# Optimization experiments

Measured on AMD Instinct MI355X. Metric: run time of the kernel, lower is better.

## Reference

```python
import jax, jax.numpy as jnp
import numpy as np

C, H, W = 32, 128, 128

def grid_sample_plane(plane, gx, gy):
    """PyTorch F.grid_sample(mode='bilinear', align_corners=True, padding_mode='zeros').
    plane: (C,H,W); gx,gy: (B,N) in [-1,1] (x indexes W, y indexes H).
    Returns (B,C,N)."""
    x = (gx + 1.0) * 0.5 * (W - 1)
    y = (gy + 1.0) * 0.5 * (H - 1)
    x0 = jnp.floor(x); y0 = jnp.floor(y)
    wx = x - x0; wy = y - y0
    x0i = x0.astype(jnp.int32); y0i = y0.astype(jnp.int32)
    def corner(xi, yi, w):
        valid = (xi >= 0) & (xi < W) & (yi >= 0) & (yi < H)
        xc = jnp.clip(xi, 0, W - 1); yc = jnp.clip(yi, 0, H - 1)
        v = plane[:, yc, xc]            # (C,B,N)
        return v * (w * valid)[None]
    out = (corner(x0i, y0i, (1 - wx) * (1 - wy))
           + corner(x0i + 1, y0i, wx * (1 - wy))
           + corner(x0i, y0i + 1, (1 - wx) * wy)
           + corner(x0i + 1, y0i + 1, wx * wy))   # (C,B,N)
    return jnp.transpose(out, (1, 0, 2))           # (B,C,N)


def setup_inputs() -> dict:
    key = jax.random.key(0)
    ks = jax.random.split(key, 8)
    B, N = 4, 262144
    grid_coords = jax.random.uniform(ks[0], (B, N, 3), jnp.float32, -1.0, 1.0)
    triplanes = jax.random.normal(ks[1], (3 * C, H, W), jnp.float32)
    w0 = jax.random.normal(ks[2], (128, 32), jnp.float32) * (1.0 / np.sqrt(32))
    b0 = jax.random.normal(ks[3], (128,), jnp.float32) * 0.01
    w1 = jax.random.normal(ks[4], (128, 128), jnp.float32) * (1.0 / np.sqrt(128))
    b1 = jax.random.normal(ks[5], (128,), jnp.float32) * 0.01
    w2 = jax.random.normal(ks[6], (4, 128), jnp.float32) * (1.0 / np.sqrt(128))
    b2 = jax.random.normal(ks[7], (4,), jnp.float32) * 0.01
    return {"grid_coords": grid_coords, "triplanes": triplanes,
            "w0": w0, "b0": b0, "w1": w1, "b1": b1, "w2": w2, "b2": b2}


def reference(grid_coords, triplanes, w0, b0, w1, b1, w2, b2):
    B, N, _ = grid_coords.shape
    feat_xy, feat_yz, feat_xz = jnp.split(triplanes, 3, axis=0)
    x = grid_coords[..., 0]; y = grid_coords[..., 1]; z = grid_coords[..., 2]
    # fused tri-plane gather + sum, (B,C,N)
    sampled = (grid_sample_plane(feat_xy, x, y)
               + grid_sample_plane(feat_xz, x, z)
               + grid_sample_plane(feat_yz, y, z))
    # NOTE: the original code does .reshape(batch, -1, channel) on a (B,C,1,N)
    # contiguous tensor (NOT a transpose) -- replicate that exact layout reinterpretation.
    feats = sampled.reshape(B, N, C)
    net = jax.nn.relu(feats @ w0.T + b0)
    net = jax.nn.relu(net @ w1.T + b1)
    net = jax.nn.relu(net @ w2.T + b2)            # (B,N,4)
    # raw = cat(rgb=net[...,1:4], alpha=net[...,0:1]) along channel
    raw = jnp.concatenate([net[..., 1:4], net[..., 0:1]], axis=-1)
    return raw
```

## Files before the change

### kernel.cpp

```cpp
#include <hip/hip_runtime.h>
#include <hip/hip_bf16.h>


#define C_ 32
#define HW_ (128 * 128)
#define HQS 40

typedef short s8v __attribute__((ext_vector_type(8)));
typedef float f4v __attribute__((ext_vector_type(4)));
typedef unsigned int u4v __attribute__((ext_vector_type(4)));
typedef unsigned int u2v __attribute__((ext_vector_type(2)));

__device__ __attribute__((aligned(64))) unsigned short g_planes[3 * HW_ * C_];
__device__ __attribute__((aligned(16))) unsigned short g_w0[128 * 32];
__device__ __attribute__((aligned(16))) unsigned short g_w1[128 * 128];
__device__ __attribute__((aligned(16))) unsigned short g_w2[16 * 128];
__device__ __attribute__((aligned(16))) float g_b0[128];
__device__ __attribute__((aligned(16))) float g_b1[128];
__device__ __attribute__((aligned(16))) float g_b2p[16];

template <typename TO, typename FROM>
static __device__ __forceinline__ TO bitc(FROM f) {
    union { FROM a; TO b; } u; u.a = f; return u.b;
}

template <typename V>
static __device__ __forceinline__ auto mfma_k32(V a, V b, f4v c, int)
    -> decltype(__builtin_amdgcn_mfma_f32_16x16x32_bf16(a, b, c, 0, 0, 0)) {
    return __builtin_amdgcn_mfma_f32_16x16x32_bf16(a, b, c, 0, 0, 0);
}
template <typename V>
static __device__ __forceinline__ f4v mfma_k32(V a, V b, f4v c, long) {
    typedef __bf16 b8v __attribute__((ext_vector_type(8)));
    return __builtin_amdgcn_mfma_f32_16x16x32_bf16(bitc<b8v>(a), bitc<b8v>(b), c, 0, 0, 0);
}
static __device__ __forceinline__ f4v MFMA(s8v a, s8v b, f4v c) {
    return mfma_k32(a, b, c, 0);
}

__device__ __forceinline__ unsigned short f2bf(float f) {
    union { float f; unsigned int i; } v; v.f = f;
    unsigned int r = v.i + 0x7FFFu + ((v.i >> 16) & 1u);
    return (unsigned short)(r >> 16);
}

static __device__ __forceinline__ unsigned int relu_pk(float a, float b) {
    float x = a > 0.0f ? a : 0.0f;
    float y = b > 0.0f ? b : 0.0f;
    unsigned int r;
    asm("v_cvt_pk_bf16_f32 %0, %1, %2" : "=v"(r) : "v"(x), "v"(y));
    return r;
}

__global__ __launch_bounds__(256) void prep_planes_k(const float* __restrict__ tp) {
    __shared__ float buf[32][65];
    const int tid = threadIdx.x;
    const int bid = blockIdx.x;
    const int pl  = bid >> 8;
    const int xy0 = (bid & 255) << 6;
#pragma unroll
    for (int i = 0; i < 8; ++i) {
        int idx = i * 256 + tid;
        int c = idx >> 6, x = idx & 63;
        buf[c][x] = tp[(pl * C_ + c) * HW_ + xy0 + x];
    }
    __syncthreads();
#pragma unroll
    for (int i = 0; i < 8; ++i) {
        int idx = i * 256 + tid;
        int x = idx >> 5, c = idx & 31;
        g_planes[(pl * HW_ + xy0 + x) * C_ + c] = f2bf(buf[c][x]);
    }
}

__global__ void prep_weights_k(const float* __restrict__ w0, const float* __restrict__ b0,
                               const float* __restrict__ w1, const float* __restrict__ b1,
                               const float* __restrict__ w2, const float* __restrict__ b2) {
    int i = blockIdx.x * 256 + threadIdx.x;
    if (i < 128 * 32)  g_w0[i] = f2bf(w0[i]);
    if (i < 128 * 128) g_w1[i] = f2bf(w1[i]);
    if (i < 16 * 128) {
        int n = i >> 7, k = i & 127;
        g_w2[i] = f2bf(n < 4 ? w2[((n + 1) & 3) * 128 + k] : 0.0f);
    }
    if (i < 128) { g_b0[i] = b0[i]; g_b1[i] = b1[i]; }
    if (i < 16)  g_b2p[i] = (i < 4) ? b2[(i + 1) & 3] : 0.0f;
}

__device__ __forceinline__ void sample_plane32(const unsigned short* __restrict__ pbase,
                                               float u, float v, float* facc) {
    float x = (u + 1.0f) * 63.5f;
    float y = (v + 1.0f) * 63.5f;
    float xf = floorf(x), yf = floorf(y);
    float wx = x - xf, wy = y - yf;
    int x0 = (int)xf, y0 = (int)yf;
#pragma unroll
    for (int dy = 0; dy < 2; ++dy) {
        int yi = y0 + dy;
        float wyv = dy ? wy : 1.0f - wy;
        bool vy = (yi >= 0) && (yi < 128);
        int yc = yi < 0 ? 0 : (yi > 127 ? 127 : yi);
#pragma unroll
        for (int dx = 0; dx < 2; ++dx) {
            int xi = x0 + dx;
            float wv = (dx ? wx : 1.0f - wx) * wyv;
            bool vx = (xi >= 0) && (xi < 128);
            int xc = xi < 0 ? 0 : (xi > 127 ? 127 : xi);
            wv = (vx && vy) ? wv : 0.0f;
            const u4v* cp = (const u4v*)(pbase + (yc * 128 + xc) * C_);
#pragma unroll
            for (int q = 0; q < 4; ++q) {
                u4v dw = cp[q];
#pragma unroll
                for (int jj = 0; jj < 4; ++jj) {
                    facc[q * 8 + 2 * jj]     += wv * __uint_as_float(dw[jj] << 16);
                    facc[q * 8 + 2 * jj + 1] += wv * __uint_as_float(dw[jj] & 0xFFFF0000u);
                }
            }
        }
    }
}

__global__ __launch_bounds__(256) void fused_k(const float* __restrict__ coords,
                                               float* __restrict__ out) {
    __shared__ __attribute__((aligned(16))) unsigned short smem[16384 + 4 * 16 * HQS];
    __shared__ __attribute__((aligned(16))) float lds_bias[256];
    const int tid  = threadIdx.x;
    const int wave = tid >> 6;
    const int lane = tid & 63;
    const int l15  = lane & 15;
    const int quad = lane >> 4;
    const int ch8  = quad * 8;

    const int wg = blockIdx.x;
    const int b  = wg >> 9;
    const int nb = wg & 511;
    const int n0 = nb << 9;

    if (tid < 128) { lds_bias[tid] = g_b0[tid]; lds_bias[128 + tid] = g_b1[tid]; }

#pragma unroll 1
    for (int pt = 0; pt < 2; ++pt) {
        const int nl = tid + pt * 256;
        const float* cp = coords + (size_t)(b * 262144 + n0 + nl) * 3;
        const float gx = cp[0], gy = cp[1], gz = cp[2];
        float facc[32];
#pragma unroll
        for (int c = 0; c < 32; ++c) facc[c] = 0.0f;
        sample_plane32(g_planes + 0 * (HW_ * C_), gx, gy, facc);
        sample_plane32(g_planes + 2 * (HW_ * C_), gx, gz, facc);
        sample_plane32(g_planes + 1 * (HW_ * C_), gy, gz, facc);
#pragma unroll
        for (int c = 0; c < 32; ++c)
            smem[c * 512 + nl] = f2bf(facc[c]);
    }
    __syncthreads();

    s8v w0f[8], w1f[4][8], w2f[4];
#pragma unroll
    for (int nt = 0; nt < 8; ++nt)
        w0f[nt] = *(const s8v*)(g_w0 + (nt * 16 + l15) * 32 + ch8);
#pragma unroll
    for (int kc = 0; kc < 4; ++kc)
#pragma unroll
        for (int nt = 0; nt < 8; ++nt)
            w1f[kc][nt] = *(const s8v*)(g_w1 + (nt * 16 + l15) * 128 + kc * 32 + ch8);
#pragma unroll
    for (int kc = 0; kc < 4; ++kc)
        w2f[kc] = *(const s8v*)(g_w2 + l15 * 128 + kc * 32 + ch8);
    const f4v b2v = *(const f4v*)(g_b2p + quad * 4);

    unsigned short* hbq = smem + 16384 + wave * (16 * HQS);

#pragma unroll 1
    for (int i = 0; i < 8; ++i) {
        const int ci = wave * 8 + i;
        int bo = 0;
        asm volatile("" : "+v"(bo));
        const float* bp = lds_bias + bo;

        const s8v a = *(const s8v*)(smem + ci * 512 + l15 * 32 + ch8);

        f4v d[8];
#pragma unroll
        for (int j = 0; j < 8; ++j)
            d[j] = *(const f4v*)(bp + 128 + j * 16 + quad * 4);

#pragma unroll
        for (int kc = 0; kc < 4; ++kc) {
#pragma unroll
            for (int s = 0; s < 2; ++s) {
                const int nt = 2 * kc + s;
                const f4v bi = *(const f4v*)(bp + nt * 16 + quad * 4);
                f4v c1 = MFMA(w0f[nt], a, bi);
                u2v pk;
                pk[0] = relu_pk(c1[0], c1[1]);
                pk[1] = relu_pk(c1[2], c1[3]);
                *(u2v*)(hbq + l15 * HQS + s * 16 + quad * 4) = pk;
            }
            const s8v a2 = *(const s8v*)(hbq + l15 * HQS + ch8);
#pragma unroll
            for (int j = 0; j < 8; ++j)
                d[j] = MFMA(w1f[kc][j], a2, d[j]);
        }

        f4v o = b2v;
#pragma unroll
        for (int kc = 0; kc < 4; ++kc) {
#pragma unroll
            for (int s = 0; s < 2; ++s) {
                const int j = 2 * kc + s;
                u2v pk;
                pk[0] = relu_pk(d[j][0], d[j][1]);
                pk[1] = relu_pk(d[j][2], d[j][3]);
                *(u2v*)(hbq + l15 * HQS + s * 16 + quad * 4) = pk;
            }
            const s8v a3 = *(const s8v*)(hbq + l15 * HQS + ch8);
            o = MFMA(w2f[kc], a3, o);
        }

        if (quad == 0) {
            f4v r;
#pragma unroll
            for (int j = 0; j < 4; ++j) r[j] = o[j] > 0.0f ? o[j] : 0.0f;
            const int t = b * 16384 + ci * 512 + nb;
            *(f4v*)(out + (size_t)(t * 16 + l15) * 4) = r;
        }
    }
}

extern "C" void kernel_launch(void* const* d_in, const int* in_sizes, int n_in,
                              void* d_out, int out_size, void* d_ws, size_t ws_size,
                              hipStream_t stream) {
    const float* coords = (const float*)d_in[0];
    const float* tp = (const float*)d_in[1];
    const float* w0 = (const float*)d_in[2];
    const float* b0 = (const float*)d_in[3];
    const float* w1 = (const float*)d_in[4];
    const float* b1 = (const float*)d_in[5];
    const float* w2 = (const float*)d_in[6];
    const float* b2 = (const float*)d_in[7];
    float* out = (float*)d_out;

    prep_planes_k<<<768, 256, 0, stream>>>(tp);
    prep_weights_k<<<64, 256, 0, stream>>>(w0, b0, w1, b1, w2, b2);
    fused_k<<<2048, 256, 0, stream>>>(coords, out);
}
```

Baseline: 214.4 us.

## Split tri-plane gather across four lanes per point with swizzled LDS layout

The gather is redistributed so four lanes cooperate on each point, each loading one 16-byte channel group per corner instead of one thread loading all 32 channels. This should coalesce corner reads into contiguous 64-byte segments and cut per-thread register use. Writes to shared memory use an XOR swizzle on the point index by channel group, and the MFMA fragment read is adjusted to match, presumably to avoid bank conflicts. The cost is that coordinate loads and bilinear weight math are now duplicated across four lanes.

```diff
diff --git a/kernel.cpp b/kernel.cpp
--- a/kernel.cpp
+++ b/kernel.cpp
@@ -87,8 +87,8 @@
     if (i < 16)  g_b2p[i] = (i < 4) ? b2[(i + 1) & 3] : 0.0f;
 }
 
-__device__ __forceinline__ void sample_plane32(const unsigned short* __restrict__ pbase,
-                                               float u, float v, float* facc) {
+__device__ __forceinline__ void sample_plane8(const unsigned short* __restrict__ pbase,
+                                              float u, float v, float* facc) {
     float x = (u + 1.0f) * 63.5f;
     float y = (v + 1.0f) * 63.5f;
     float xf = floorf(x), yf = floorf(y);
@@ -107,15 +107,11 @@
             bool vx = (xi >= 0) && (xi < 128);
             int xc = xi < 0 ? 0 : (xi > 127 ? 127 : xi);
             wv = (vx && vy) ? wv : 0.0f;
-            const u4v* cp = (const u4v*)(pbase + (yc * 128 + xc) * C_);
-#pragma unroll
-            for (int q = 0; q < 4; ++q) {
-                u4v dw = cp[q];
-#pragma unroll
-                for (int jj = 0; jj < 4; ++jj) {
-                    facc[q * 8 + 2 * jj]     += wv * __uint_as_float(dw[jj] << 16);
-                    facc[q * 8 + 2 * jj + 1] += wv * __uint_as_float(dw[jj] & 0xFFFF0000u);
-                }
+            const u4v dw = *(const u4v*)(pbase + (yc * 128 + xc) * C_);
+#pragma unroll
+            for (int jj = 0; jj < 4; ++jj) {
+                facc[2 * jj]     += wv * __uint_as_float(dw[jj] << 16);
+                facc[2 * jj + 1] += wv * __uint_as_float(dw[jj] & 0xFFFF0000u);
             }
         }
     }
@@ -139,20 +135,28 @@
 
     if (tid < 128) { lds_bias[tid] = g_b0[tid]; lds_bias[128 + tid] = g_b1[tid]; }
 
+    {
+        const int qa  = lane & 3;
+        const int p15 = lane >> 2;
+        const unsigned short* pb0 = g_planes + 0 * (HW_ * C_) + qa * 8;
+        const unsigned short* pb1 = g_planes + 1 * (HW_ * C_) + qa * 8;
+        const unsigned short* pb2 = g_planes + 2 * (HW_ * C_) + qa * 8;
 #pragma unroll 1
-    for (int pt = 0; pt < 2; ++pt) {
-        const int nl = tid + pt * 256;
-        const float* cp = coords + (size_t)(b * 262144 + n0 + nl) * 3;
-        const float gx = cp[0], gy = cp[1], gz = cp[2];
-        float facc[32];
-#pragma unroll
-        for (int c = 0; c < 32; ++c) facc[c] = 0.0f;
-        sample_plane32(g_planes + 0 * (HW_ * C_), gx, gy, facc);
-        sample_plane32(g_planes + 2 * (HW_ * C_), gx, gz, facc);
-        sample_plane32(g_planes + 1 * (HW_ * C_), gy, gz, facc);
-#pragma unroll
-        for (int c = 0; c < 32; ++c)
-            smem[c * 512 + nl] = f2bf(facc[c]);
+        for (int s = 0; s < 8; ++s) {
+            const int nl = s * 64 + wave * 16 + p15;
+            const float* cp = coords + (size_t)(b * 262144 + n0 + nl) * 3;
+            const float gx = cp[0], gy = cp[1], gz = cp[2];
+            float facc[8];
+#pragma unroll
+            for (int j = 0; j < 8; ++j) facc[j] = 0.0f;
+            sample_plane8(pb0, gx, gy, facc);
+            sample_plane8(pb2, gx, gz, facc);
+            sample_plane8(pb1, gy, gz, facc);
+            const int nlx = nl ^ (qa << 4);
+#pragma unroll
+            for (int j = 0; j < 8; ++j)
+                smem[(qa * 8 + j) * 512 + nlx] = f2bf(facc[j]);
+        }
     }
     __syncthreads();
 
@@ -171,6 +175,7 @@
     const f4v b2v = *(const f4v*)(g_b2p + quad * 4);
 
     unsigned short* hbq = smem + 16384 + wave * (16 * HQS);
+    const int xw = wave << 4;
 
 #pragma unroll 1
     for (int i = 0; i < 8; ++i) {
@@ -179,7 +184,7 @@
         asm volatile("" : "+v"(bo));
         const float* bp = lds_bias + bo;
 
-        const s8v a = *(const s8v*)(smem + ci * 512 + l15 * 32 + ch8);
+        const s8v a = *(const s8v*)(smem + ci * 512 + ((l15 * 32 + ch8) ^ xw));
 
         f4v d[8];
 #pragma unroll
```

Measured after the change: 206.1 us. 1.04x faster.
